# Kernel optimization log

Measured on AMD Instinct MI355X. Metric: run time of the kernel, lower is better.

Reference implementation:

```python
import jax, jax.numpy as jnp
import numpy as np


def setup_inputs() -> dict:
    key = jax.random.key(0)
    B, C, H, W = 8, 512, 64, 64
    x = jax.random.normal(key, (B, C, H, W), dtype=jnp.float32)
    # flag: 1 = masked (hole) position, 0 = known. Center-square hole as in
    # mask to this resolution; with shift_sz=1, mask_thred=1 flag == mask).
    flag = np.zeros((H, W), dtype=np.int32)
    flag[H // 4: 3 * H // 4, W // 4: 3 * W // 4] = 1
    return {"input": x, "flag": jnp.asarray(flag)}


def reference(input, flag):
    B, C, H, W = input.shape
    c2 = C // 2
    hw = H * W
    former = input[:, :c2]          # decoder features (B, c2, H, W)
    latter = input[:, c2:]          # encoder features (B, c2, H, W)

    ff = former.reshape(B, c2, hw)  # (B, c2, P)
    lf = latter.reshape(B, c2, hw)  # (B, c2, P)

    # L2-normalize latter pixel features (shift_sz=1 patches == pixels);
    # matches util.cosine_similarity's normalized conv kernels.
    norms = jnp.linalg.norm(lf, axis=1, keepdims=True)
    lnorm = lf / jnp.maximum(norms, 1e-8)

    # cosine[b, p, q] = <former[b,:,p], normed_latter[b,:,q]> for all positions;
    # masked q are excluded from the argmax (equiv. to gathering only the
    # non-mask patches via nonmask_point_idx, but jit-friendly fixed shapes).
    cos = jnp.einsum('bcp,bcq->bpq', ff, lnorm)
    flag_f = flag.reshape(hw)
    neg_inf = jnp.asarray(-jnp.inf, cos.dtype)
    cos = jnp.where(flag_f[None, None, :] == 1, neg_inf, cos)

    idx = jnp.argmax(cos, axis=2)   # (B, P): best non-mask source per position

    # Gather RAW latter features at best-match positions (util.shift_offsets
    # applies the 0/1 transition matrix ind_lst to the un-normalized latter).
    gidx = jnp.broadcast_to(idx[:, None, :], (B, c2, hw))
    shift = jnp.take_along_axis(lf, gidx, axis=2)            # (B, c2, P)
    shift = jnp.where(flag_f[None, None, :] == 1, shift, 0.0)  # zeros at known px
    shift = shift.reshape(B, c2, H, W)

    return jnp.concatenate([former, latter, shift], axis=1)   # (B, 3*c2, H, W)
```

## Files before the change

### kernel.cpp

```cpp
#include <hip/hip_runtime.h>
#include <stdint.h>
#include <math.h>

#define HW   4096
#define NB   8
#define NC   512
#define C2   256
#define PT   32
#define QC   256
#define NCHK 16

#define WS_PACKED 0
#define WS_Q0     393216
#define WS_P1     409600
#define WS_CNT    425984
#define WS_INVC   558080

__device__ __forceinline__ unsigned long long mkkey(float v, unsigned q) {
    unsigned u = __float_as_uint(v);
    u = (u & 0x80000000u) ? ~u : (u | 0x80000000u);
    return ((unsigned long long)u << 32) | (unsigned long long)(0xFFFFFFFFu - q);
}

__device__ __forceinline__ float* lfc_region(float* out, int b) {
    return out + ((size_t)b * 768 + 512) * HW;
}

__global__ void compact_kernel(const int* __restrict__ flag, int* __restrict__ q0,
                               int* __restrict__ p1, int* __restrict__ cnt) {
    __shared__ int c1s[256];
    int t = threadIdx.x;
    int f[16]; int n1 = 0;
    #pragma unroll
    for (int j = 0; j < 16; ++j) { f[j] = flag[t*16 + j]; n1 += (f[j] == 1); }
    c1s[t] = n1;
    __syncthreads();
    if (t == 0) {
        int run = 0;
        for (int i = 0; i < 256; ++i) { int v = c1s[i]; c1s[i] = run; run += v; }
        cnt[0] = run;
        cnt[1] = HW - run;
    }
    __syncthreads();
    int b1 = c1s[t];
    int b0 = t*16 - c1s[t];
    for (int j = 0; j < 16; ++j) {
        int i = t*16 + j;
        if (f[j] == 1) p1[b1++] = i; else q0[b0++] = i;
    }
}

__global__ void pack_kernel(const float* __restrict__ x,
                            const int* __restrict__ q0, const int* __restrict__ p1,
                            const int* __restrict__ cnt, float* __restrict__ out) {
    int b = blockIdx.z, cy = blockIdx.y;
    int i = blockIdx.x * 256 + threadIdx.x;
    int n1 = cnt[0], n0 = cnt[1];
    int ns = (n0 + 3) & ~3, ms = (n1 + 3) & ~3;
    const float* xrow = x + ((size_t)b * NC + cy) * HW;
    out[((size_t)b * 768 + cy) * HW + i] = xrow[i];
    if (cy < C2) {
        if (i < n1) {
            float* ffc = lfc_region(out, b) + (size_t)C2 * ns;
            ffc[(size_t)cy * ms + i] = xrow[p1[i]];
        }
    } else {
        int c = cy - C2;
        if (i < n0) {
            float* lfc = lfc_region(out, b);
            lfc[(size_t)c * ns + i] = xrow[q0[i]];
        }
    }
}

__global__ void invc_kernel(const float* __restrict__ out, const int* __restrict__ cnt,
                            float* __restrict__ invc) {
    int b = blockIdx.y;
    int n0 = cnt[1];
    int ns = (n0 + 3) & ~3;
    int k = blockIdx.x * 256 + threadIdx.x;
    if (k >= n0) return;
    const float* lfc = lfc_region((float*)out, b) + k;
    float s = 0.f;
    #pragma unroll 8
    for (int c = 0; c < C2; ++c) {
        float v = lfc[(size_t)c * ns];
        s = fmaf(v, v, s);
    }
    invc[b * HW + k] = 1.0f / fmaxf(sqrtf(s), 1e-8f);
}

__global__ void __launch_bounds__(256) argmax_kernel(
        float* __restrict__ out, const float* __restrict__ invc,
        const int* __restrict__ q0, const int* __restrict__ p1,
        const int* __restrict__ cnt, unsigned long long* __restrict__ packed) {
    int bid   = blockIdx.x;
    int b     = bid & 7;
    int s     = bid >> 3;
    int chunk = s >> 5;
    int tile  = s & 31;
    int n1 = cnt[0], n0 = cnt[1];
    if (tile * PT >= n1) return;
    if (chunk * QC >= n0) return;
    int ns = (n0 + 3) & ~3, ms = (n1 + 3) & ~3;

    __shared__ float sff[128][PT];

    int t = threadIdx.x;
    int tp = t >> 6;
    int tq = t & 63;

    const float* lfc = lfc_region(out, b);
    const float* ffc = lfc + (size_t)C2 * ns;
    int kbase = chunk * QC + tq * 4;

    const float* r = lfc + kbase;
    float4 f0 = *(const float4*)(r);
    float4 f1 = *(const float4*)(r + ns);

    float acc[8][4];
    #pragma unroll
    for (int pi = 0; pi < 8; ++pi)
        #pragma unroll
        for (int j = 0; j < 4; ++j) acc[pi][j] = 0.f;

    bool fulltile = (tile * PT + PT <= n1);

    for (int h = 0; h < 2; ++h) {
        __syncthreads();
        if (fulltile) {
            #pragma unroll
            for (int k = 0; k < 4; ++k) {
                int i4 = t + (k << 8);
                int c = i4 >> 3, jg = i4 & 7;
                ((float4*)sff)[i4] =
                    *(const float4*)&ffc[(size_t)(h * 128 + c) * ms + tile * PT + jg * 4];
            }
        } else {
            #pragma unroll
            for (int k = 0; k < 4; ++k) {
                int i4 = t + (k << 8);
                int c = i4 >> 3, jg = i4 & 7;
                const float* src = &ffc[(size_t)(h * 128 + c) * ms];
                int m0 = tile * PT + jg * 4;
                float4 v;
                v.x = (m0 + 0 < n1) ? src[m0 + 0] : 0.f;
                v.y = (m0 + 1 < n1) ? src[m0 + 1] : 0.f;
                v.z = (m0 + 2 < n1) ? src[m0 + 2] : 0.f;
                v.w = (m0 + 3 < n1) ? src[m0 + 3] : 0.f;
                ((float4*)sff)[i4] = v;
            }
        }
        __syncthreads();

        #pragma unroll 2
        for (int cc = 0; cc < 128; cc += 2) {
            float4 f2 = *(const float4*)(r + 2 * (size_t)ns);
            {
                const float4* arow = (const float4*)&sff[cc][tp * 8];
                float4 a0 = arow[0], a1 = arow[1];
                float av[8] = {a0.x, a0.y, a0.z, a0.w, a1.x, a1.y, a1.z, a1.w};
                #pragma unroll
                for (int pi = 0; pi < 8; ++pi) {
                    acc[pi][0] = fmaf(av[pi], f0.x, acc[pi][0]);
                    acc[pi][1] = fmaf(av[pi], f0.y, acc[pi][1]);
                    acc[pi][2] = fmaf(av[pi], f0.z, acc[pi][2]);
                    acc[pi][3] = fmaf(av[pi], f0.w, acc[pi][3]);
                }
            }
            float4 f3 = *(const float4*)(r + 3 * (size_t)ns);
            {
                const float4* arow = (const float4*)&sff[cc + 1][tp * 8];
                float4 a0 = arow[0], a1 = arow[1];
                float av[8] = {a0.x, a0.y, a0.z, a0.w, a1.x, a1.y, a1.z, a1.w};
                #pragma unroll
                for (int pi = 0; pi < 8; ++pi) {
                    acc[pi][0] = fmaf(av[pi], f1.x, acc[pi][0]);
                    acc[pi][1] = fmaf(av[pi], f1.y, acc[pi][1]);
                    acc[pi][2] = fmaf(av[pi], f1.z, acc[pi][2]);
                    acc[pi][3] = fmaf(av[pi], f1.w, acc[pi][3]);
                }
            }
            f0 = f2; f1 = f3;
            r += 2 * (size_t)ns;
        }
    }

    float best[8];
    int   bq[8];
    #pragma unroll
    for (int pi = 0; pi < 8; ++pi) { best[pi] = -INFINITY; bq[pi] = 0x7FFFFFFF; }

    #pragma unroll
    for (int j = 0; j < 4; ++j) {
        int k = kbase + j;
        if (k >= n0) continue;
        float sc = invc[b * HW + k];
        int   q  = q0[k];
        #pragma unroll
        for (int pi = 0; pi < 8; ++pi) {
            float cv = acc[pi][j] * sc;
            if (cv > best[pi] || (cv == best[pi] && q < bq[pi])) {
                best[pi] = cv; bq[pi] = q;
            }
        }
    }

    #pragma unroll
    for (int m = 1; m < 64; m <<= 1) {
        #pragma unroll
        for (int pi = 0; pi < 8; ++pi) {
            float ov = __shfl_xor(best[pi], m);
            int   oq = __shfl_xor(bq[pi], m);
            if (ov > best[pi] || (ov == best[pi] && oq < bq[pi])) {
                best[pi] = ov; bq[pi] = oq;
            }
        }
    }
    if (tq == 0) {
        #pragma unroll
        for (int pi = 0; pi < 8; ++pi) {
            int pidx = tile * PT + tp * 8 + pi;
            int p = (pidx < n1) ? p1[pidx] : -1;
            if (p >= 0)
                atomicMax(&packed[(size_t)b * HW + p], mkkey(best[pi], (unsigned)bq[pi]));
        }
    }
}

__global__ void shift_kernel(const float* __restrict__ x, const int* __restrict__ flag,
                             const unsigned long long* __restrict__ packed,
                             float* __restrict__ out) {
    int cc = blockIdx.x, b = blockIdx.y;
    const float* lfrow = x + ((size_t)b * NC + C2 + cc) * HW;
    float*       orow  = out + ((size_t)b * 768 + 512 + cc) * HW;
    const unsigned long long* pk = packed + (size_t)b * HW;
    for (int p = threadIdx.x; p < HW; p += 256) {
        float v = 0.f;
        if (flag[p] == 1) {
            unsigned low = (unsigned)(pk[p] & 0xFFFFFFFFull);
            int q = (int)((0xFFFFFFFFu - low) & (HW - 1));
            v = lfrow[q];
        }
        orow[p] = v;
    }
}

extern "C" void kernel_launch(void* const* d_in, const int* in_sizes, int n_in,
                              void* d_out, int out_size, void* d_ws, size_t ws_size,
                              hipStream_t stream) {
    const float* x    = (const float*)d_in[0];
    const int*   flag = (const int*)d_in[1];
    float*       out  = (float*)d_out;
    char*        ws   = (char*)d_ws;

    unsigned long long* packed = (unsigned long long*)(ws + WS_PACKED);
    int*   q0   = (int*)(ws + WS_Q0);
    int*   p1   = (int*)(ws + WS_P1);
    int*   cnt  = (int*)(ws + WS_CNT);
    float* invc = (float*)(ws + WS_INVC);

    hipMemsetAsync(packed, 0, (size_t)NB * HW * sizeof(unsigned long long), stream);

    compact_kernel<<<1, 256, 0, stream>>>(flag, q0, p1, cnt);
    pack_kernel<<<dim3(HW / 256, NC, NB), 256, 0, stream>>>(x, q0, p1, cnt, out);
    invc_kernel<<<dim3(HW / 256, NB), 256, 0, stream>>>(out, cnt, invc);
    argmax_kernel<<<dim3(NB * NCHK * 32), 256, 0, stream>>>(out, invc, q0, p1, cnt, packed);
    shift_kernel<<<dim3(C2, NB), 256, 0, stream>>>(x, flag, packed, out);
}
```

Measured before the change: 264.1 us.

## Process two q-chunks per argmax block and deepen register prefetch

Each argmax block now loops over two consecutive q-chunks, halving the grid and merging the per-thread best/index before the single warp reduction and atomic write. The inner channel loop keeps four prefetched float4 rows of latter features in flight instead of two. The aim is fewer atomics and less block overhead, plus better hiding of global load latency. The cost is fewer blocks for occupancy and a reload of the former-feature tile for every chunk.

Result: slower. 271.9 us (+3.0%).

```diff
diff --git a/kernel.cpp b/kernel.cpp
--- a/kernel.cpp
+++ b/kernel.cpp
@@ -8,7 +8,7 @@
 #define C2   256
 #define PT   32
 #define QC   256
-#define NCHK 16
+#define NPAIR 8
 
 #define WS_PACKED 0
 #define WS_Q0     393216
@@ -90,6 +90,18 @@
     invc[b * HW + k] = 1.0f / fmaxf(sqrtf(s), 1e-8f);
 }
 
+#define ROWFMA(CC, F) {                                                   \
+    const float4* arow = (const float4*)&sff[CC][tp * 8];                 \
+    float4 a0 = arow[0], a1 = arow[1];                                    \
+    float av[8] = {a0.x, a0.y, a0.z, a0.w, a1.x, a1.y, a1.z, a1.w};       \
+    _Pragma("unroll")                                                     \
+    for (int pi = 0; pi < 8; ++pi) {                                      \
+        acc[pi][0] = fmaf(av[pi], F.x, acc[pi][0]);                       \
+        acc[pi][1] = fmaf(av[pi], F.y, acc[pi][1]);                       \
+        acc[pi][2] = fmaf(av[pi], F.z, acc[pi][2]);                       \
+        acc[pi][3] = fmaf(av[pi], F.w, acc[pi][3]);                       \
+    } }
+
 __global__ void __launch_bounds__(256) argmax_kernel(
         float* __restrict__ out, const float* __restrict__ invc,
         const int* __restrict__ q0, const int* __restrict__ p1,
@@ -97,11 +109,11 @@
     int bid   = blockIdx.x;
     int b     = bid & 7;
     int s     = bid >> 3;
-    int chunk = s >> 5;
+    int pair  = s >> 5;
     int tile  = s & 31;
     int n1 = cnt[0], n0 = cnt[1];
     if (tile * PT >= n1) return;
-    if (chunk * QC >= n0) return;
+    if (pair * 2 * QC >= n0) return;
     int ns = (n0 + 3) & ~3, ms = (n1 + 3) & ~3;
 
     __shared__ float sff[128][PT];
@@ -112,96 +124,75 @@
 
     const float* lfc = lfc_region(out, b);
     const float* ffc = lfc + (size_t)C2 * ns;
-    int kbase = chunk * QC + tq * 4;
-
-    const float* r = lfc + kbase;
-    float4 f0 = *(const float4*)(r);
-    float4 f1 = *(const float4*)(r + ns);
-
-    float acc[8][4];
-    #pragma unroll
-    for (int pi = 0; pi < 8; ++pi)
-        #pragma unroll
-        for (int j = 0; j < 4; ++j) acc[pi][j] = 0.f;
-
     bool fulltile = (tile * PT + PT <= n1);
-
-    for (int h = 0; h < 2; ++h) {
-        __syncthreads();
-        if (fulltile) {
-            #pragma unroll
-            for (int k = 0; k < 4; ++k) {
-                int i4 = t + (k << 8);
-                int c = i4 >> 3, jg = i4 & 7;
-                ((float4*)sff)[i4] =
-                    *(const float4*)&ffc[(size_t)(h * 128 + c) * ms + tile * PT + jg * 4];
-            }
-        } else {
-            #pragma unroll
-            for (int k = 0; k < 4; ++k) {
-                int i4 = t + (k << 8);
-                int c = i4 >> 3, jg = i4 & 7;
-                const float* src = &ffc[(size_t)(h * 128 + c) * ms];
-                int m0 = tile * PT + jg * 4;
-                float4 v;
-                v.x = (m0 + 0 < n1) ? src[m0 + 0] : 0.f;
-                v.y = (m0 + 1 < n1) ? src[m0 + 1] : 0.f;
-                v.z = (m0 + 2 < n1) ? src[m0 + 2] : 0.f;
-                v.w = (m0 + 3 < n1) ? src[m0 + 3] : 0.f;
-                ((float4*)sff)[i4] = v;
-            }
-        }
-        __syncthreads();
-
-        #pragma unroll 2
-        for (int cc = 0; cc < 128; cc += 2) {
-            float4 f2 = *(const float4*)(r + 2 * (size_t)ns);
-            {
-                const float4* arow = (const float4*)&sff[cc][tp * 8];
-                float4 a0 = arow[0], a1 = arow[1];
-                float av[8] = {a0.x, a0.y, a0.z, a0.w, a1.x, a1.y, a1.z, a1.w};
-                #pragma unroll
-                for (int pi = 0; pi < 8; ++pi) {
-                    acc[pi][0] = fmaf(av[pi], f0.x, acc[pi][0]);
-                    acc[pi][1] = fmaf(av[pi], f0.y, acc[pi][1]);
-                    acc[pi][2] = fmaf(av[pi], f0.z, acc[pi][2]);
-                    acc[pi][3] = fmaf(av[pi], f0.w, acc[pi][3]);
-                }
-            }
-            float4 f3 = *(const float4*)(r + 3 * (size_t)ns);
-            {
-                const float4* arow = (const float4*)&sff[cc + 1][tp * 8];
-                float4 a0 = arow[0], a1 = arow[1];
-                float av[8] = {a0.x, a0.y, a0.z, a0.w, a1.x, a1.y, a1.z, a1.w};
-                #pragma unroll
-                for (int pi = 0; pi < 8; ++pi) {
-                    acc[pi][0] = fmaf(av[pi], f1.x, acc[pi][0]);
-                    acc[pi][1] = fmaf(av[pi], f1.y, acc[pi][1]);
-                    acc[pi][2] = fmaf(av[pi], f1.z, acc[pi][2]);
-                    acc[pi][3] = fmaf(av[pi], f1.w, acc[pi][3]);
-                }
-            }
-            f0 = f2; f1 = f3;
-            r += 2 * (size_t)ns;
-        }
-    }
 
     float best[8];
     int   bq[8];
     #pragma unroll
     for (int pi = 0; pi < 8; ++pi) { best[pi] = -INFINITY; bq[pi] = 0x7FFFFFFF; }
 
-    #pragma unroll
-    for (int j = 0; j < 4; ++j) {
-        int k = kbase + j;
-        if (k >= n0) continue;
-        float sc = invc[b * HW + k];
-        int   q  = q0[k];
-        #pragma unroll
-        for (int pi = 0; pi < 8; ++pi) {
-            float cv = acc[pi][j] * sc;
-            if (cv > best[pi] || (cv == best[pi] && q < bq[pi])) {
-                best[pi] = cv; bq[pi] = q;
+    for (int chunk = pair * 2; chunk < pair * 2 + 2 && chunk * QC < n0; ++chunk) {
+        int kbase = chunk * QC + tq * 4;
+        const float* r = lfc + kbase;
+        float4 f0 = *(const float4*)(r);
+        float4 f1 = *(const float4*)(r + (size_t)ns);
+        float4 f2 = *(const float4*)(r + 2 * (size_t)ns);
+        float4 f3 = *(const float4*)(r + 3 * (size_t)ns);
+
+        float acc[8][4];
+        #pragma unroll
+        for (int pi = 0; pi < 8; ++pi)
+            #pragma unroll
+            for (int j = 0; j < 4; ++j) acc[pi][j] = 0.f;
+
+        for (int h = 0; h < 2; ++h) {
+            __syncthreads();
+            if (fulltile) {
+                #pragma unroll
+                for (int k = 0; k < 4; ++k) {
+                    int i4 = t + (k << 8);
+                    int c = i4 >> 3, jg = i4 & 7;
+                    ((float4*)sff)[i4] =
+                        *(const float4*)&ffc[(size_t)(h * 128 + c) * ms + tile * PT + jg * 4];
+                }
+            } else {
+                #pragma unroll
+                for (int k = 0; k < 4; ++k) {
+                    int i4 = t + (k << 8);
+                    int c = i4 >> 3, jg = i4 & 7;
+                    const float* src = &ffc[(size_t)(h * 128 + c) * ms];
+                    int m0 = tile * PT + jg * 4;
+                    float4 v;
+                    v.x = (m0 + 0 < n1) ? src[m0 + 0] : 0.f;
+                    v.y = (m0 + 1 < n1) ? src[m0 + 1] : 0.f;
+                    v.z = (m0 + 2 < n1) ? src[m0 + 2] : 0.f;
+                    v.w = (m0 + 3 < n1) ? src[m0 + 3] : 0.f;
+                    ((float4*)sff)[i4] = v;
+                }
+            }
+            __syncthreads();
+
+            for (int cc = 0; cc < 128; cc += 4) {
+                ROWFMA(cc,     f0); f0 = *(const float4*)(r + 4 * (size_t)ns);
+                ROWFMA(cc + 1, f1); f1 = *(const float4*)(r + 5 * (size_t)ns);
+                ROWFMA(cc + 2, f2); f2 = *(const float4*)(r + 6 * (size_t)ns);
+                ROWFMA(cc + 3, f3); f3 = *(const float4*)(r + 7 * (size_t)ns);
+                r += 4 * (size_t)ns;
+            }
+        }
+
+        #pragma unroll
+        for (int j = 0; j < 4; ++j) {
+            int k = kbase + j;
+            if (k >= n0) continue;
+            float sc = invc[b * HW + k];
+            int   q  = q0[k];
+            #pragma unroll
+            for (int pi = 0; pi < 8; ++pi) {
+                float cv = acc[pi][j] * sc;
+                if (cv > best[pi] || (cv == best[pi] && q < bq[pi])) {
+                    best[pi] = cv; bq[pi] = q;
+                }
             }
         }
     }
@@ -265,6 +256,6 @@
     compact_kernel<<<1, 256, 0, stream>>>(flag, q0, p1, cnt);
     pack_kernel<<<dim3(HW / 256, NC, NB), 256, 0, stream>>>(x, q0, p1, cnt, out);
     invc_kernel<<<dim3(HW / 256, NB), 256, 0, stream>>>(out, cnt, invc);
-    argmax_kernel<<<dim3(NB * NCHK * 32), 256, 0, stream>>>(out, invc, q0, p1, cnt, packed);
+    argmax_kernel<<<dim3(NB * NPAIR * 32), 256, 0, stream>>>(out, invc, q0, p1, cnt, packed);
     shift_kernel<<<dim3(C2, NB), 256, 0, stream>>>(x, flag, packed, out);
 }
```
